# Performance work log

Hardware: AMD Instinct MI355X
Metric: run time of the kernel (lower is better)

Reference implementation:

```python
import jax, jax.numpy as jnp
import numpy as np

B, H, W = 8, 64, 64
DIM1, DIM2 = 384, 256
NH, DH = 8, 32
INNER = NH * DH
EPS = 1e-5


def _layernorm(x, w, b):
    mu = jnp.mean(x, axis=-1, keepdims=True)
    var = jnp.mean((x - mu) ** 2, axis=-1, keepdims=True)
    return (x - mu) * jax.lax.rsqrt(var + EPS) * w + b


def _axial_attn(q, k, v, scale):
    # q,k,v: [B,H,W,nh,dh]; row attention over H, col attention over W
    sh = jnp.einsum('biwnd,bjwnd->bwnij', q, k) * scale  # [B,W,nh,H,H]
    oh = jnp.einsum('bwnij,bjwnd->biwnd', jax.nn.softmax(sh, axis=-1), v)
    sw = jnp.einsum('bhind,bhjnd->bhnij', q, k) * scale  # [B,H,nh,W,W]
    ow = jnp.einsum('bhnij,bhjnd->bhind', jax.nn.softmax(sw, axis=-1), v)
    return oh + ow  # [B,H,W,nh,dh]


def setup_inputs() -> dict:
    key = jax.random.key(0)
    ks = jax.random.split(key, 16)
    s1 = 1.0 / np.sqrt(DIM1)
    s2 = 1.0 / np.sqrt(DIM2)
    si = 1.0 / np.sqrt(INNER)
    return {
        'x1': jax.random.normal(ks[0], (B, DIM1, H, W), jnp.float32),
        'x2': jax.random.normal(ks[1], (B, DIM2, H, W), jnp.float32),
        'ln1q_w': jnp.ones((DIM1,), jnp.float32),
        'ln1q_b': jnp.zeros((DIM1,), jnp.float32),
        'ln2kv_w': jnp.ones((DIM2,), jnp.float32),
        'ln2kv_b': jnp.zeros((DIM2,), jnp.float32),
        'Wq1': jax.random.normal(ks[2], (DIM1, INNER), jnp.float32) * s1,
        'Wkv2': jax.random.normal(ks[3], (DIM2, 2 * INNER), jnp.float32) * s2,
        'Wout1': jax.random.normal(ks[4], (INNER, DIM2), jnp.float32) * si,
        'bout1': jnp.zeros((DIM2,), jnp.float32),
        'ln2q_w': jnp.ones((DIM2,), jnp.float32),
        'ln2q_b': jnp.zeros((DIM2,), jnp.float32),
        'ln1kv_w': jnp.ones((DIM1,), jnp.float32),
        'ln1kv_b': jnp.zeros((DIM1,), jnp.float32),
        'Wq2': jax.random.normal(ks[5], (DIM2, INNER), jnp.float32) * s2,
        'Wkv1': jax.random.normal(ks[6], (DIM1, 2 * INNER), jnp.float32) * s1,
        'Wout2': jax.random.normal(ks[7], (INNER, DIM2), jnp.float32) * si,
        'bout2': jnp.zeros((DIM2,), jnp.float32),
        'Wsc': jax.random.normal(ks[8], (DIM2, DIM1), jnp.float32) * s1,  # 1x1 conv [out,in]
        'bn_gamma': jnp.ones((DIM2,), jnp.float32),
        'bn_beta': jnp.zeros((DIM2,), jnp.float32),
        'bn_mean': jnp.zeros((DIM2,), jnp.float32),
        'bn_var': jnp.ones((DIM2,), jnp.float32),
    }


def reference(x1, x2, ln1q_w, ln1q_b, ln2kv_w, ln2kv_b, Wq1, Wkv2, Wout1, bout1,
              ln2q_w, ln2q_b, ln1kv_w, ln1kv_b, Wq2, Wkv1, Wout2, bout2,
              Wsc, bn_gamma, bn_beta, bn_mean, bn_var):
    b, c1, h, w = x1.shape
    scale = DH ** -0.5
    x1f = jnp.transpose(x1, (0, 2, 3, 1))  # [B,H,W,C1]
    x2f = jnp.transpose(x2, (0, 2, 3, 1))  # [B,H,W,C2]

    def heads(t):
        return t.reshape(b, h, w, NH, DH)

    # branch 1: q from x1, kv from x2
    q1 = _layernorm(x1f, ln1q_w, ln1q_b) @ Wq1
    kv2 = _layernorm(x2f, ln2kv_w, ln2kv_b) @ Wkv2
    k2, v2 = jnp.split(kv2, 2, axis=-1)
    o1 = _axial_attn(heads(q1), heads(k2), heads(v2), scale)
    fused1 = o1.reshape(b, h, w, INNER) @ Wout1 + bout1
    # shortcut: 1x1 conv + BN (inference stats)
    sc = jnp.einsum('bhwc,oc->bhwo', x1f, Wsc)
    sc = (sc - bn_mean) * jax.lax.rsqrt(bn_var + EPS) * bn_gamma + bn_beta
    y1 = sc + fused1

    # branch 2: q from x2, kv from x1
    q2 = _layernorm(x2f, ln2q_w, ln2q_b) @ Wq2
    kv1 = _layernorm(x1f, ln1kv_w, ln1kv_b) @ Wkv1
    k1, v1 = jnp.split(kv1, 2, axis=-1)
    o2 = _axial_attn(heads(q2), heads(k1), heads(v1), scale)
    fused2 = o2.reshape(b, h, w, INNER) @ Wout2 + bout2
    y2 = x2f + fused2

    out = y1 + y2  # [B,H,W,C2]
    return jnp.transpose(out, (0, 3, 1, 2))
```

## Files before the change

kernel.cpp:

```cpp
#include <hip/hip_runtime.h>

typedef unsigned short u16;
typedef unsigned int u32;
typedef float v4f __attribute__((ext_vector_type(4)));
typedef __bf16 v8bf __attribute__((ext_vector_type(8)));

__device__ __forceinline__ float bf2f(u16 v) {
  union { u32 u; float f; } x; x.u = ((u32)v) << 16; return x.f;
}
__device__ __forceinline__ u16 f2bf(float f) {
  union { float f; u32 u; } x; x.f = f;
  u32 u = x.u;
  return (u16)((u + 0x7FFFu + ((u >> 16) & 1u)) >> 16);
}
__device__ __forceinline__ u32 f2u(float f) {
  union { float f; u32 u; } x; x.f = f; return x.u;
}
__device__ __forceinline__ u32 pk2bf(float a, float b) {
  const u32 au = f2u(a) + 0x8000u;
  const u32 bu = f2u(b) + 0x8000u;
  return (bu & 0xFFFF0000u) | (au >> 16);
}

struct Ptrs { const void* p[23]; };

__global__ __launch_bounds__(256) void convert_all(Ptrs ps, u16* __restrict__ cx1,
                                                   u16* __restrict__ cx2,
                                                   u16* __restrict__ cw) {
  static const int sz[23]  = {12582912, 8388608, 384, 384, 256, 256, 98304, 131072,
                              65536, 256, 256, 256, 384, 384, 65536, 196608, 65536,
                              256, 98304, 256, 256, 256, 256};
  static const int off[23] = {0, 0, 0, 384, 768, 1024, 1280, 99584, 230656, 296192,
                              296448, 296704, 296960, 297344, 297728, 363264, 559872,
                              625408, 625664, 723968, 724224, 724480, 724736};
  const int ti = blockIdx.y;
  const int n8 = sz[ti] >> 3;
  const bool isf32 = (((const u32*)ps.p[2])[0] == 0x3F800000u);
  u16* dst = (ti == 0) ? cx1 : (ti == 1) ? cx2 : (cw + off[ti]);
  const void* src = ps.p[ti];
  const int stride = gridDim.x * blockDim.x;
  for (int i = blockIdx.x * blockDim.x + threadIdx.x; i < n8; i += stride) {
    if (isf32) {
      const float4 f0 = ((const float4*)src)[2*i];
      const float4 f1 = ((const float4*)src)[2*i + 1];
      u16 tmp[8];
      tmp[0] = f2bf(f0.x); tmp[1] = f2bf(f0.y); tmp[2] = f2bf(f0.z); tmp[3] = f2bf(f0.w);
      tmp[4] = f2bf(f1.x); tmp[5] = f2bf(f1.y); tmp[6] = f2bf(f1.z); tmp[7] = f2bf(f1.w);
      ((uint4*)dst)[i] = *(const uint4*)tmp;
    } else {
      ((uint4*)dst)[i] = ((const uint4*)src)[i];
    }
  }
}

__global__ void prep_bt(const u16* __restrict__ lnq_w, const u16* __restrict__ lnq_b,
                        const u16* __restrict__ lnkv_w, const u16* __restrict__ lnkv_b,
                        const u16* __restrict__ Wq, const u16* __restrict__ Wkv,
                        u16* __restrict__ BT, float* __restrict__ bias) {
  const int C = blockDim.x;
  const int j = blockIdx.x;
  const int c = threadIdx.x;
  float w, bco, wv;
  if (j < 256) { w = bf2f(lnq_w[c]); bco = bf2f(lnq_b[c]); wv = bf2f(Wq[c*256 + j]); }
  else         { w = bf2f(lnkv_w[c]); bco = bf2f(lnkv_b[c]); wv = bf2f(Wkv[c*512 + (j-256)]); }
  BT[(size_t)j*C + c] = f2bf(w * wv);
  __shared__ float red[384];
  red[c] = bco * wv;
  __syncthreads();
  if (c == 0) { float s = 0.f; for (int i = 0; i < C; i++) s += red[i]; bias[j] = s; }
}

__global__ void prep_fin(const u16* __restrict__ Wout1, const u16* __restrict__ Wout2,
                         const u16* __restrict__ Wsc, const u16* __restrict__ bout1,
                         const u16* __restrict__ bout2, const u16* __restrict__ gam,
                         const u16* __restrict__ bet, const u16* __restrict__ mean,
                         const u16* __restrict__ var, u16* __restrict__ BT,
                         float* __restrict__ bias) {
  const int o = blockIdx.x, t = threadIdx.x;
  const float g = rsqrtf(bf2f(var[o]) + 1e-5f) * bf2f(gam[o]);
  for (int idx = t; idx < 1408; idx += 256) {
    float v;
    if (idx < 512)       v = bf2f(Wout1[(idx & 255)*256 + o]);
    else if (idx < 1024) v = bf2f(Wout2[((idx - 512) & 255)*256 + o]);
    else                 v = bf2f(Wsc[o*384 + (idx - 1024)]) * g;
    BT[(size_t)o*1408 + idx] = f2bf(v);
  }
  if (t == 0) bias[o] = bf2f(bet[o]) - bf2f(mean[o])*g + bf2f(bout1[o]) + bf2f(bout2[o]);
}

__global__ __launch_bounds__(256) void ln_c384(const u16* __restrict__ x,
                                               u16* __restrict__ xn, u16* __restrict__ xraw) {
  __shared__ u16 tile[384*66];
  __shared__ float rsum[4][64], rsq[4][64], smean[64], srstd[64];
  const int t = threadIdx.x, w = t & 63, g = t >> 6;
  const int bh = blockIdx.x, b = bh >> 6, h = bh & 63;
  const u16* src = x + (size_t)b*384*4096 + h*64 + w;
  float sum = 0.f, sq = 0.f;
  for (int j = 0; j < 96; j++) {
    const int c = g*96 + j;
    const u16 uv = src[(size_t)c*4096];
    tile[c*66 + w] = uv;
    const float v = bf2f(uv); sum += v; sq += v*v;
  }
  rsum[g][w] = sum; rsq[g][w] = sq;
  __syncthreads();
  if (t < 64) {
    const float s = rsum[0][t]+rsum[1][t]+rsum[2][t]+rsum[3][t];
    const float q = rsq[0][t]+rsq[1][t]+rsq[2][t]+rsq[3][t];
    const float mean = s * (1.0f/384.0f);
    float var = q * (1.0f/384.0f) - mean*mean;
    if (var < 0.f) var = 0.f;
    smean[t] = mean; srstd[t] = rsqrtf(var + 1e-5f);
  }
  __syncthreads();
  const size_t pos0 = (size_t)bh * 64;
  for (int i = 0; i < 96; i++) {
    const int flat = i*256 + t;
    const int ww = flat / 384, c = flat - ww*384;
    const u16 uv = tile[c*66 + ww];
    const float v = (bf2f(uv) - smean[ww]) * srstd[ww];
    const size_t p = pos0 + ww;
    xn[p*384 + c] = f2bf(v);
    xraw[p*384 + c] = uv;
  }
}

__global__ __launch_bounds__(256) void ln_c256(const u16* __restrict__ x,
                                               u16* __restrict__ xn) {
  __shared__ u16 tile[256*66];
  __shared__ float rsum[4][64], rsq[4][64], smean[64], srstd[64];
  const int t = threadIdx.x, w = t & 63, g = t >> 6;
  const int bh = blockIdx.x, b = bh >> 6, h = bh & 63;
  const u16* src = x + (size_t)b*256*4096 + h*64 + w;
  float sum = 0.f, sq = 0.f;
  for (int j = 0; j < 64; j++) {
    const int c = g*64 + j;
    const u16 uv = src[(size_t)c*4096];
    tile[c*66 + w] = uv;
    const float v = bf2f(uv); sum += v; sq += v*v;
  }
  rsum[g][w] = sum; rsq[g][w] = sq;
  __syncthreads();
  if (t < 64) {
    const float s = rsum[0][t]+rsum[1][t]+rsum[2][t]+rsum[3][t];
    const float q = rsq[0][t]+rsq[1][t]+rsq[2][t]+rsq[3][t];
    const float mean = s * (1.0f/256.0f);
    float var = q * (1.0f/256.0f) - mean*mean;
    if (var < 0.f) var = 0.f;
    smean[t] = mean; srstd[t] = rsqrtf(var + 1e-5f);
  }
  __syncthreads();
  const size_t pos0 = (size_t)bh * 64;
  for (int i = 0; i < 64; i++) {
    const int flat = i*256 + t;
    const int ww = flat >> 8, c = flat & 255;
    const float v = (bf2f(tile[c*66 + ww]) - smean[ww]) * srstd[ww];
    xn[(pos0 + ww)*256 + c] = f2bf(v);
  }
}

__global__ __launch_bounds__(256) void gemm_bt(const u16* __restrict__ A,
                                               const u16* __restrict__ BT,
                                               u16* __restrict__ C,
                                               const float* __restrict__ bias,
                                               int N, int K) {
  __shared__ u16 lsA[128*40];
  __shared__ u16 lsB[128*40];
  const int t = threadIdx.x;
  const int m0 = blockIdx.x * 128, n0 = blockIdx.y * 128;
  const int lane = t & 63, wv = t >> 6;
  const int wm = wv & 1, wn = wv >> 1;
  const int lo = lane & 15, hi = lane >> 4;
  const int r0 = t >> 2, c8 = (t & 3) << 3;
  const u16* Ab = A + (size_t)(m0 + r0) * K + c8;
  const u16* Bb = BT + (size_t)(n0 + r0) * K + c8;
  uint4 a0 = *(const uint4*)(Ab);
  uint4 a1 = *(const uint4*)(Ab + (size_t)64*K);
  uint4 b0 = *(const uint4*)(Bb);
  uint4 b1 = *(const uint4*)(Bb + (size_t)64*K);
  v4f acc[4][4] = {};
  for (int kb = 0; kb < K; kb += 32) {
    __syncthreads();
    *(uint4*)&lsA[r0*40 + c8] = a0;
    *(uint4*)&lsA[(r0+64)*40 + c8] = a1;
    *(uint4*)&lsB[r0*40 + c8] = b0;
    *(uint4*)&lsB[(r0+64)*40 + c8] = b1;
    __syncthreads();
    if (kb + 32 < K) {
      a0 = *(const uint4*)(Ab + kb + 32);
      a1 = *(const uint4*)(Ab + (size_t)64*K + kb + 32);
      b0 = *(const uint4*)(Bb + kb + 32);
      b1 = *(const uint4*)(Bb + (size_t)64*K + kb + 32);
    }
    v8bf av[4], bv[4];
#pragma unroll
    for (int i = 0; i < 4; i++) av[i] = *(const v8bf*)&lsA[(wm*64 + i*16 + lo)*40 + hi*8];
#pragma unroll
    for (int i = 0; i < 4; i++) bv[i] = *(const v8bf*)&lsB[(wn*64 + i*16 + lo)*40 + hi*8];
#pragma unroll
    for (int mt = 0; mt < 4; mt++)
#pragma unroll
      for (int nt = 0; nt < 4; nt++)
        acc[mt][nt] = __builtin_amdgcn_mfma_f32_16x16x32_bf16(av[mt], bv[nt], acc[mt][nt], 0, 0, 0);
  }
#pragma unroll
  for (int mt = 0; mt < 4; mt++) {
    const int row = m0 + wm*64 + mt*16 + hi*4;
#pragma unroll
    for (int nt = 0; nt < 4; nt++) {
      const int col = n0 + wn*64 + nt*16 + lo;
      const float bs = bias[col];
#pragma unroll
      for (int r = 0; r < 4; r++)
        C[(size_t)(row + r) * N + col] = f2bf(acc[mt][nt][r] + bs);
    }
  }
}

__global__ __launch_bounds__(512) void gemm_final(const u16* __restrict__ Ao,
                                                  const u16* __restrict__ Ar,
                                                  const u16* __restrict__ BT,
                                                  const float* __restrict__ bias,
                                                  const u16* __restrict__ x2c,
                                                  const u32* __restrict__ probe,
                                                  void* __restrict__ outv) {
  __shared__ u16 smem[16640];
  u16* lsA = smem;
  u16* lsB = smem + 5120;
  const int t = threadIdx.x;
  const int m0 = blockIdx.x * 128, n0 = blockIdx.y * 128;
  const int lane = t & 63, wv = t >> 6;
  const int wm = wv >> 1, wn = wv & 1;
  const int lo = lane & 15, hi = lane >> 4;
  const int r0 = t >> 2, c8 = (t & 3) << 3;
  const u16* ArR = Ar + (size_t)(m0 + r0) * 384 + c8;
  const u16* Bb  = BT + (size_t)(n0 + r0) * 1408 + c8;

  uint4 a, bq;
  {
    a = *(const uint4*)(Ao + ((size_t)(0) * 32768 + m0 + r0) * 32 + c8);
    bq = *(const uint4*)(Bb);
  }
  v4f acc[2][4] = {};
  for (int kb = 0; kb < 1408; kb += 32) {
    __syncthreads();
    *(uint4*)&lsA[r0*40 + c8] = a;
    *(uint4*)&lsB[r0*40 + c8] = bq;
    __syncthreads();
    const int kn = kb + 32;
    if (kn < 1408) {
      if (kn < 1024) a = *(const uint4*)(Ao + ((size_t)(kn >> 5) * 32768 + m0 + r0) * 32 + c8);
      else           a = *(const uint4*)(ArR + (kn - 1024));
      bq = *(const uint4*)(Bb + kn);
    }
    v8bf av[2], bv[4];
#pragma unroll
    for (int i = 0; i < 2; i++) av[i] = *(const v8bf*)&lsA[(wm*32 + i*16 + lo)*40 + hi*8];
#pragma unroll
    for (int i = 0; i < 4; i++) bv[i] = *(const v8bf*)&lsB[(wn*64 + i*16 + lo)*40 + hi*8];
#pragma unroll
    for (int mt = 0; mt < 2; mt++)
#pragma unroll
      for (int nt = 0; nt < 4; nt++)
        acc[mt][nt] = __builtin_amdgcn_mfma_f32_16x16x32_bf16(av[mt], bv[nt], acc[mt][nt], 0, 0, 0);
  }
  __syncthreads();
#pragma unroll
  for (int mt = 0; mt < 2; mt++)
#pragma unroll
    for (int nt = 0; nt < 4; nt++) {
      const int nl = wn*64 + nt*16 + lo;
      const float bs = bias[n0 + nl];
#pragma unroll
      for (int r = 0; r < 4; r++)
        smem[(wm*32 + mt*16 + hi*4 + r)*130 + nl] = f2bf(acc[mt][nt][r] + bs);
    }
  __syncthreads();
  const bool isf32 = (probe[0] == 0x3F800000u);
  const int bh0 = blockIdx.x * 2;
  for (int i = 0; i < 32; i++) {
    const int flat = i*512 + t;
    const int nl = flat >> 7;
    const int rem = flat & 127;
    const int mb = rem >> 6, w = rem & 63;
    const int bh = bh0 + mb, b = bh >> 6, h = bh & 63;
    const size_t oidx = ((size_t)(b*256 + n0 + nl)*64 + h)*64 + w;
    const float val = bf2f(smem[(mb*64 + w)*130 + nl]) + bf2f(x2c[oidx]);
    if (isf32) ((float*)outv)[oidx] = val;
    else       ((u16*)outv)[oidx]   = f2bf(val);
  }
}

__global__ __launch_bounds__(512) void attn(const u16* __restrict__ qkv1,
                                            const u16* __restrict__ qkv2,
                                            u16* __restrict__ Ao) {
  __shared__ __attribute__((aligned(16))) u16 smem[8 * 2560];
  const int t = threadIdx.x;
  const int head = t >> 6, lane = t & 63;
  const int lo = lane & 15, quad = lane >> 4;
  u16* sw = smem + head * 2560;
  const int bx = blockIdx.x;
  const int z = blockIdx.y;
  const int br = z >> 1, dir = z & 1;
  const int b = bx >> 6, x = bx & 63;
  const u16* Qb  = (br == 0) ? qkv1 : qkv2;
  const u16* KVb = (br == 0) ? qkv2 : qkv1;
  const int qc = head*32, kc = 256 + head*32, vc = 512 + head*32;
  const int pbase = (dir == 0) ? (b*4096 + x) : ((b*64 + x)*64);
  const int pstr  = (dir == 0) ? 64 : 1;

  {
    const u16* vr = KVb + (size_t)(pbase + lane*pstr)*768 + vc;
    u16 vbuf[32];
#pragma unroll
    for (int i = 0; i < 4; i++) *(uint4*)&vbuf[i*8] = *(const uint4*)(vr + i*8);
    const int khi = lane >> 3, klo = lane & 7;
#pragma unroll
    for (int d = 0; d < 32; d++)
      sw[d*64 + ((khi ^ (d & 7)) << 3) + klo] = vbuf[d];
  }
  __syncthreads();

  v8bf qa[4], ka[4];
#pragma unroll
  for (int i = 0; i < 4; i++) {
    const size_t p = (size_t)(pbase + (i*16 + lo)*pstr) * 768;
    qa[i] = *(const v8bf*)(Qb + p + qc + quad*8);
    ka[i] = *(const v8bf*)(KVb + p + kc + quad*8);
  }

  v4f s[4][4];
#pragma unroll
  for (int qt = 0; qt < 4; qt++)
#pragma unroll
    for (int kt = 0; kt < 4; kt++) {
      v4f z4 = {};
      s[qt][kt] = __builtin_amdgcn_mfma_f32_16x16x32_bf16(ka[kt], qa[qt], z4, 0, 0, 0);
    }

  v8bf va[2][2];
#pragma unroll
  for (int mt = 0; mt < 2; mt++)
#pragma unroll
    for (int ks = 0; ks < 2; ks++) {
      const int d = mt*16 + lo;
      va[mt][ks] = *(const v8bf*)&sw[d*64 + (((ks*4 + quad) ^ (d & 7)) << 3)];
    }

  const float scale = 0.17677669529663687f;
  v4f o[2][4] = {};
#pragma unroll
  for (int qt = 0; qt < 4; qt++) {
    float tv[16];
    float mx = -1e30f;
#pragma unroll
    for (int kt = 0; kt < 4; kt++)
#pragma unroll
      for (int r = 0; r < 4; r++) {
        const float v = s[qt][kt][r] * scale;
        tv[kt*4 + r] = v;
        mx = fmaxf(mx, v);
      }
    mx = fmaxf(mx, __shfl_xor(mx, 16));
    mx = fmaxf(mx, __shfl_xor(mx, 32));
    float sm = 0.f;
#pragma unroll
    for (int i = 0; i < 16; i++) { tv[i] = __expf(tv[i] - mx); sm += tv[i]; }
    sm += __shfl_xor(sm, 16);
    sm += __shfl_xor(sm, 32);
    const float inv = 1.0f / sm;
    u32 pk[4][2];
#pragma unroll
    for (int kt = 0; kt < 4; kt++)
#pragma unroll
      for (int rp = 0; rp < 2; rp++)
        pk[kt][rp] = pk2bf(tv[kt*4 + rp*2] * inv, tv[kt*4 + rp*2 + 1] * inv);
    u32 pw[2][4];
#pragma unroll
    for (int ks = 0; ks < 2; ks++)
#pragma unroll
      for (int rp = 0; rp < 2; rp++) {
        const u32 v16 = (quad < 2)  ? pk[2*ks][rp]   : pk[2*ks+1][rp];
        const u32 v32 = (quad < 2)  ? pk[2*ks+1][rp] : pk[2*ks][rp];
        const u32 v48 = (quad & 1)  ? pk[2*ks+1][rp] : pk[2*ks][rp];
        const u32 r16 = (u32)__shfl_xor((int)v16, 16);
        const u32 r32 = (u32)__shfl_xor((int)v32, 32);
        const u32 r48 = (u32)__shfl_xor((int)v48, 48);
        const u32 wlo = (quad == 0) ? pk[2*ks][rp] : (quad == 1) ? r48 : (quad == 2) ? r32 : r16;
        const u32 whi = (quad == 0) ? r16 : (quad == 1) ? r32 : (quad == 2) ? r48 : pk[2*ks+1][rp];
        pw[ks][rp] = wlo;
        pw[ks][2 + rp] = whi;
      }
#pragma unroll
    for (int ks = 0; ks < 2; ks++) {
      union { u32 u[4]; v8bf v; } pb;
      pb.u[0] = pw[ks][0]; pb.u[1] = pw[ks][1]; pb.u[2] = pw[ks][2]; pb.u[3] = pw[ks][3];
#pragma unroll
      for (int mt = 0; mt < 2; mt++)
        o[mt][qt] = __builtin_amdgcn_mfma_f32_16x16x32_bf16(va[mt][ks], pb.v, o[mt][qt], 0, 0, 0);
    }
  }

  __syncthreads();
#pragma unroll
  for (int mt = 0; mt < 2; mt++)
#pragma unroll
    for (int nt = 0; nt < 4; nt++)
#pragma unroll
      for (int rp = 0; rp < 2; rp++) {
        const u32 pkv = pk2bf(o[mt][nt][rp*2], o[mt][nt][rp*2 + 1]);
        *(u32*)&sw[(nt*16 + lo)*40 + mt*16 + quad*4 + rp*2] = pkv;
      }
  __syncthreads();
  {
    const size_t sbase = (size_t)(z*8 + head) * 32768 + pbase;
#pragma unroll
    for (int it = 0; it < 4; it++) {
      const int chunk = it*64 + lane;
      const int row = chunk >> 2, ic = chunk & 3;
      *(uint4*)&Ao[(sbase + (size_t)row*pstr)*32 + ic*8] = *(const uint4*)&sw[row*40 + ic*8];
    }
  }
}

extern "C" void kernel_launch(void* const* d_in, const int* in_sizes, int n_in,
                              void* d_out, int out_size, void* d_ws, size_t ws_size,
                              hipStream_t stream) {
  char* ws = (char*)d_ws;
  u16* Ao    = (u16*)(ws);
  u16* Araw  = (u16*)(ws + 67108864);
  u16* qkv1  = (u16*)(ws + 92274688);
  u16* qkv2  = (u16*)(ws + 142606336);
  u16* cx2   = (u16*)(ws + 192937984);
  u16* cw    = (u16*)(ws + 209715200);
  u16* BT1   = (u16*)(ws + 211165184);
  u16* BT2   = (u16*)(ws + 211755008);
  u16* BTf   = (u16*)(ws + 212148224);
  float* bias1 = (float*)(ws + 212869120);
  float* bias2 = (float*)(ws + 212872192);
  float* biasf = (float*)(ws + 212875264);
  u16* cx1 = qkv1;
  u16* x1n = Ao;
  u16* x2n = Ao + 12582912;

  u16* c_ln1q_w = cw + 0,     *c_ln1q_b = cw + 384;
  u16* c_ln2kv_w = cw + 768,  *c_ln2kv_b = cw + 1024;
  u16* c_Wq1 = cw + 1280,     *c_Wkv2 = cw + 99584;
  u16* c_Wout1 = cw + 230656, *c_bout1 = cw + 296192;
  u16* c_ln2q_w = cw + 296448,*c_ln2q_b = cw + 296704;
  u16* c_ln1kv_w = cw + 296960,*c_ln1kv_b = cw + 297344;
  u16* c_Wq2 = cw + 297728,   *c_Wkv1 = cw + 363264;
  u16* c_Wout2 = cw + 559872, *c_bout2 = cw + 625408;
  u16* c_Wsc = cw + 625664;
  u16* c_bn_g = cw + 723968,  *c_bn_b = cw + 724224;
  u16* c_bn_m = cw + 724480,  *c_bn_v = cw + 724736;

  Ptrs ps;
  for (int i = 0; i < 23; i++) ps.p[i] = d_in[i];

  convert_all<<<dim3(512, 23), 256, 0, stream>>>(ps, cx1, cx2, cw);
  prep_bt<<<768, 384, 0, stream>>>(c_ln1q_w, c_ln1q_b, c_ln1kv_w, c_ln1kv_b, c_Wq1, c_Wkv1, BT1, bias1);
  prep_bt<<<768, 256, 0, stream>>>(c_ln2q_w, c_ln2q_b, c_ln2kv_w, c_ln2kv_b, c_Wq2, c_Wkv2, BT2, bias2);
  prep_fin<<<256, 256, 0, stream>>>(c_Wout1, c_Wout2, c_Wsc, c_bout1, c_bout2,
                                    c_bn_g, c_bn_b, c_bn_m, c_bn_v, BTf, biasf);
  ln_c384<<<512, 256, 0, stream>>>(cx1, x1n, Araw);
  ln_c256<<<512, 256, 0, stream>>>(cx2, x2n);
  gemm_bt<<<dim3(256, 6), 256, 0, stream>>>(x1n, BT1, qkv1, bias1, 768, 384);
  gemm_bt<<<dim3(256, 6), 256, 0, stream>>>(x2n, BT2, qkv2, bias2, 768, 256);
  attn<<<dim3(512, 4), 512, 0, stream>>>(qkv1, qkv2, Ao);
  gemm_final<<<dim3(256, 2), 512, 0, stream>>>(Ao, Araw, BTf, biasf, cx2,
                                               (const u32*)d_in[2], d_out);
}
```

Measured before the change: 358.9 us.

## Use 16x16x16 MFMA for PV to drop shuffles, defer softmax normalization

Switches the attention P·V product from 16x16x32 to 16x16x16 bf16 MFMA so the score accumulator layout feeds the B operand directly. This removes the cross-lane shuffle permutation of P. Softmax normalization moves after the PV matmul, and exp is computed via exp2 with the log2e factor folded into the scale. It also adds s_setprio around the MFMA sections and changes pk2bf to round-to-nearest-even, which costs a few extra ALU ops per conversion. The change trades cheaper data movement for twice as many, smaller MFMA instructions.

```diff
diff --git a/kernel.cpp b/kernel.cpp
--- a/kernel.cpp
+++ b/kernel.cpp
@@ -4,6 +4,7 @@
 typedef unsigned int u32;
 typedef float v4f __attribute__((ext_vector_type(4)));
 typedef __bf16 v8bf __attribute__((ext_vector_type(8)));
+typedef short v4s __attribute__((ext_vector_type(4)));
 
 __device__ __forceinline__ float bf2f(u16 v) {
   union { u32 u; float f; } x; x.u = ((u32)v) << 16; return x.f;
@@ -17,9 +18,19 @@
   union { float f; u32 u; } x; x.f = f; return x.u;
 }
 __device__ __forceinline__ u32 pk2bf(float a, float b) {
-  const u32 au = f2u(a) + 0x8000u;
-  const u32 bu = f2u(b) + 0x8000u;
+  const u32 au = f2u(a) + 0x7FFFu + ((f2u(a) >> 16) & 1u);
+  const u32 bu = f2u(b) + 0x7FFFu + ((f2u(b) >> 16) & 1u);
   return (bu & 0xFFFF0000u) | (au >> 16);
+}
+
+__device__ __forceinline__ v4f mfma16(v4s a, v4s b, v4f c) {
+#if __has_builtin(__builtin_amdgcn_mfma_f32_16x16x16bf16_1k)
+  return __builtin_amdgcn_mfma_f32_16x16x16bf16_1k(a, b, c, 0, 0, 0);
+#else
+  v4f d = c;
+  asm volatile("v_mfma_f32_16x16x16_bf16 %0, %1, %2, %0" : "+v"(d) : "v"(a), "v"(b));
+  return d;
+#endif
 }
 
 struct Ptrs { const void* p[23]; };
@@ -330,6 +341,7 @@
   }
 
   v4f s[4][4];
+  __builtin_amdgcn_s_setprio(1);
 #pragma unroll
   for (int qt = 0; qt < 4; qt++)
 #pragma unroll
@@ -337,18 +349,20 @@
       v4f z4 = {};
       s[qt][kt] = __builtin_amdgcn_mfma_f32_16x16x32_bf16(ka[kt], qa[qt], z4, 0, 0, 0);
     }
-
-  v8bf va[2][2];
+  __builtin_amdgcn_s_setprio(0);
+
+  v4s va16[2][4];
 #pragma unroll
   for (int mt = 0; mt < 2; mt++)
 #pragma unroll
-    for (int ks = 0; ks < 2; ks++) {
+    for (int kt = 0; kt < 4; kt++) {
       const int d = mt*16 + lo;
-      va[mt][ks] = *(const v8bf*)&sw[d*64 + (((ks*4 + quad) ^ (d & 7)) << 3)];
-    }
-
-  const float scale = 0.17677669529663687f;
+      va16[mt][kt] = *(const v4s*)&sw[d*64 + (((2*kt + (quad >> 1)) ^ (d & 7)) << 3) + (quad & 1)*4];
+    }
+
+  const float scale2 = 0.25503483f;
   v4f o[2][4] = {};
+  float inv4[4];
 #pragma unroll
   for (int qt = 0; qt < 4; qt++) {
     float tv[16];
@@ -357,7 +371,7 @@
     for (int kt = 0; kt < 4; kt++)
 #pragma unroll
       for (int r = 0; r < 4; r++) {
-        const float v = s[qt][kt][r] * scale;
+        const float v = s[qt][kt][r] * scale2;
         tv[kt*4 + r] = v;
         mx = fmaxf(mx, v);
       }
@@ -365,50 +379,31 @@
     mx = fmaxf(mx, __shfl_xor(mx, 32));
     float sm = 0.f;
 #pragma unroll
-    for (int i = 0; i < 16; i++) { tv[i] = __expf(tv[i] - mx); sm += tv[i]; }
+    for (int i = 0; i < 16; i++) { tv[i] = exp2f(tv[i] - mx); sm += tv[i]; }
     sm += __shfl_xor(sm, 16);
     sm += __shfl_xor(sm, 32);
-    const float inv = 1.0f / sm;
-    u32 pk[4][2];
-#pragma unroll
-    for (int kt = 0; kt < 4; kt++)
-#pragma unroll
-      for (int rp = 0; rp < 2; rp++)
-        pk[kt][rp] = pk2bf(tv[kt*4 + rp*2] * inv, tv[kt*4 + rp*2 + 1] * inv);
-    u32 pw[2][4];
-#pragma unroll
-    for (int ks = 0; ks < 2; ks++)
+    inv4[qt] = 1.0f / sm;
+    __builtin_amdgcn_s_setprio(1);
+#pragma unroll
+    for (int kt = 0; kt < 4; kt++) {
+      union { u32 u[2]; v4s v; } pb;
+      pb.u[0] = pk2bf(tv[kt*4 + 0], tv[kt*4 + 1]);
+      pb.u[1] = pk2bf(tv[kt*4 + 2], tv[kt*4 + 3]);
+#pragma unroll
+      for (int mt = 0; mt < 2; mt++)
+        o[mt][qt] = mfma16(va16[mt][kt], pb.v, o[mt][qt]);
+    }
+    __builtin_amdgcn_s_setprio(0);
+  }
+
+  __syncthreads();
+#pragma unroll
+  for (int mt = 0; mt < 2; mt++)
+#pragma unroll
+    for (int nt = 0; nt < 4; nt++)
 #pragma unroll
       for (int rp = 0; rp < 2; rp++) {
-        const u32 v16 = (quad < 2)  ? pk[2*ks][rp]   : pk[2*ks+1][rp];
-        const u32 v32 = (quad < 2)  ? pk[2*ks+1][rp] : pk[2*ks][rp];
-        const u32 v48 = (quad & 1)  ? pk[2*ks+1][rp] : pk[2*ks][rp];
-        const u32 r16 = (u32)__shfl_xor((int)v16, 16);
-        const u32 r32 = (u32)__shfl_xor((int)v32, 32);
-        const u32 r48 = (u32)__shfl_xor((int)v48, 48);
-        const u32 wlo = (quad == 0) ? pk[2*ks][rp] : (quad == 1) ? r48 : (quad == 2) ? r32 : r16;
-        const u32 whi = (quad == 0) ? r16 : (quad == 1) ? r32 : (quad == 2) ? r48 : pk[2*ks+1][rp];
-        pw[ks][rp] = wlo;
-        pw[ks][2 + rp] = whi;
-      }
-#pragma unroll
-    for (int ks = 0; ks < 2; ks++) {
-      union { u32 u[4]; v8bf v; } pb;
-      pb.u[0] = pw[ks][0]; pb.u[1] = pw[ks][1]; pb.u[2] = pw[ks][2]; pb.u[3] = pw[ks][3];
-#pragma unroll
-      for (int mt = 0; mt < 2; mt++)
-        o[mt][qt] = __builtin_amdgcn_mfma_f32_16x16x32_bf16(va[mt][ks], pb.v, o[mt][qt], 0, 0, 0);
-    }
-  }
-
-  __syncthreads();
-#pragma unroll
-  for (int mt = 0; mt < 2; mt++)
-#pragma unroll
-    for (int nt = 0; nt < 4; nt++)
-#pragma unroll
-      for (int rp = 0; rp < 2; rp++) {
-        const u32 pkv = pk2bf(o[mt][nt][rp*2], o[mt][nt][rp*2 + 1]);
+        const u32 pkv = pk2bf(o[mt][nt][rp*2] * inv4[nt], o[mt][nt][rp*2 + 1] * inv4[nt]);
         *(u32*)&sw[(nt*16 + lo)*40 + mt*16 + quad*4 + rp*2] = pkv;
       }
   __syncthreads();
```

Result: no change. 353.6 us (-1.5%).
